# Optimization experiments

Hardware: AMD Instinct MI355X
Metric: run time of the kernel (lower is better)

Reference implementation:

```python
import jax, jax.numpy as jnp
import numpy as np


def sobel_kernels_3d(dtype=jnp.float32):
    # Standard 3D Sobel: derivative [-1,0,1] along one axis, smoothing [1,2,1]
    # along the other two. Returns shape (3, 1, 3, 3, 3) in OIDHW layout.
    s = jnp.array([1.0, 2.0, 1.0], dtype=dtype)
    d = jnp.array([-1.0, 0.0, 1.0], dtype=dtype)
    kd = jnp.einsum('i,j,k->ijk', d, s, s)  # d/dD
    kh = jnp.einsum('i,j,k->ijk', s, d, s)  # d/dH
    kw = jnp.einsum('i,j,k->ijk', s, s, d)  # d/dW
    return jnp.stack([kd, kh, kw], axis=0)[:, None]  # (3,1,3,3,3)


def _grad3d(x, kernels):
    # x: (B, C, D, H, W) -> flatten (B*C, 1, D, H, W), conv with padding=1.
    B, C, D, H, W = x.shape
    x_ = x.reshape(B * C, 1, D, H, W)
    return jax.lax.conv_general_dilated(
        x_, kernels.astype(x.dtype),
        window_strides=(1, 1, 1),
        padding=((1, 1), (1, 1), (1, 1)),
        dimension_numbers=('NCDHW', 'OIDHW', 'NCDHW'),
    )  # (B*C, 3, D, H, W)


def setup_inputs() -> dict:
    key = jax.random.key(0)
    k1, k2 = jax.random.split(key)
    shape = (4, 4, 64, 128, 128)
    pred = jax.random.normal(k1, shape, dtype=jnp.float32)
    target = jax.random.normal(k2, shape, dtype=jnp.float32)
    return {"pred": pred, "target": target}


def reference(pred, target):
    kernels = sobel_kernels_3d(pred.dtype)
    grad_pred = _grad3d(pred, kernels)
    grad_target = _grad3d(target, kernels)
    # loss_type == 'l1'
    return jnp.mean(jnp.abs(grad_pred - grad_target))
```

## Files before the change

### kernel.cpp

```cpp
#include <hip/hip_runtime.h>

#define NB 16
#define DD 64
#define HH 128
#define WW 128

constexpr int TH = 8;
constexpr int CD = 8;
constexpr int LY = TH + 2;
constexpr float INV_COUNT = 1.0f / 50331648.0f;

__global__ void zero_out_kernel(float* out) {
    if (threadIdx.x == 0 && blockIdx.x == 0) out[0] = 0.0f;
}

__global__ __launch_bounds__(256) void sobel_l1_kernel(
    const float* __restrict__ pred,
    const float* __restrict__ target,
    float* __restrict__ out)
{
    __shared__ float buf[2][LY * WW];
    __shared__ float wsum[4];

    const int tid = threadIdx.x;
    int b = blockIdx.x;
    const int bh = b & 15; b >>= 4;
    const int bc = b & 7;  b >>= 3;
    const int bn = b;

    const int h0 = bh * TH;
    const int d0 = bc * CD;
    const size_t nbase = (size_t)bn * (DD * HH * WW);

    const int tc  = tid & 31;
    const int lh  = tid >> 5;

    auto load_plane = [&](int gd, float4& v0, float4& v1) {
        v0 = float4{0.f, 0.f, 0.f, 0.f};
        v1 = float4{0.f, 0.f, 0.f, 0.f};
        if ((unsigned)gd < DD) {
            const size_t pbase = nbase + (size_t)gd * (HH * WW);
            const int gh = h0 - 1 + lh;
            if ((unsigned)gh < HH) {
                const size_t idx = pbase + (size_t)gh * WW + 4 * tc;
                const float4 p = *(const float4*)(pred + idx);
                const float4 q = *(const float4*)(target + idx);
                v0 = float4{p.x - q.x, p.y - q.y, p.z - q.z, p.w - q.w};
            }
            if (tid < 64) {
                const int gh2 = h0 - 1 + 8 + lh;
                if ((unsigned)gh2 < HH) {
                    const size_t idx = pbase + (size_t)gh2 * WW + 4 * tc;
                    const float4 p = *(const float4*)(pred + idx);
                    const float4 q = *(const float4*)(target + idx);
                    v1 = float4{p.x - q.x, p.y - q.y, p.z - q.z, p.w - q.w};
                }
            }
        }
    };

    auto store_plane = [&](int p, const float4& v0, const float4& v1) {
        float* B = buf[p];
        *(float4*)&B[lh * WW + 4 * tc] = v0;
        if (tid < 64)
            *(float4*)&B[(8 + lh) * WW + 4 * tc] = v1;
    };

    auto partial = [&](int p, float4& A_, float4& Bh_, float4& Bw_) {
        const float* B = buf[p];
        float4 rs[3], rdw[3];
#pragma unroll
        for (int r = 0; r < 3; ++r) {
            const float4 q = *(const float4*)&B[(lh + r) * WW + 4 * tc];
            float lm = __shfl_up(q.w, 1, 32);
            float rp = __shfl_down(q.x, 1, 32);
            if (tc == 0)  lm = 0.f;
            if (tc == 31) rp = 0.f;
            rs[r]  = float4{lm  + 2.f * q.x + q.y,
                            q.x + 2.f * q.y + q.z,
                            q.y + 2.f * q.z + q.w,
                            q.z + 2.f * q.w + rp};
            rdw[r] = float4{q.y - lm, q.z - q.x, q.w - q.y, rp - q.z};
        }
        A_  = float4{rs[0].x + 2.f * rs[1].x + rs[2].x,
                     rs[0].y + 2.f * rs[1].y + rs[2].y,
                     rs[0].z + 2.f * rs[1].z + rs[2].z,
                     rs[0].w + 2.f * rs[1].w + rs[2].w};
        Bh_ = float4{rs[2].x - rs[0].x, rs[2].y - rs[0].y,
                     rs[2].z - rs[0].z, rs[2].w - rs[0].w};
        Bw_ = float4{rdw[0].x + 2.f * rdw[1].x + rdw[2].x,
                     rdw[0].y + 2.f * rdw[1].y + rdw[2].y,
                     rdw[0].z + 2.f * rdw[1].z + rdw[2].z,
                     rdw[0].w + 2.f * rdw[1].w + rdw[2].w};
    };

    float4 rA[3], rBh[3], rBw[3];
    {
        float4 a0, a1, b0v, b1v;
        load_plane(d0 - 1, a0, a1);
        load_plane(d0,     b0v, b1v);
        store_plane(0, a0, a1);
        store_plane(1, b0v, b1v);
        __syncthreads();
        partial(0, rA[0], rBh[0], rBw[0]);
        partial(1, rA[1], rBh[1], rBw[1]);
    }

    float acc = 0.0f;
#pragma unroll
    for (int ld = 0; ld < CD; ++ld) {
        float4 c0, c1;
        load_plane(d0 + ld + 1, c0, c1);
        __syncthreads();
        store_plane(ld & 1, c0, c1);
        __syncthreads();
        const int s0 = ld % 3, s1 = (ld + 1) % 3, s2 = (ld + 2) % 3;
        partial(ld & 1, rA[s2], rBh[s2], rBw[s2]);

        const float4 a0 = rA[s0],  a2 = rA[s2];
        const float4 b0 = rBh[s0], b1 = rBh[s1], b2 = rBh[s2];
        const float4 c0v = rBw[s0], c1v = rBw[s1], c2v = rBw[s2];
        acc += fabsf(a2.x - a0.x) + fabsf(a2.y - a0.y)
             + fabsf(a2.z - a0.z) + fabsf(a2.w - a0.w);
        acc += fabsf(b0.x + 2.f * b1.x + b2.x) + fabsf(b0.y + 2.f * b1.y + b2.y)
             + fabsf(b0.z + 2.f * b1.z + b2.z) + fabsf(b0.w + 2.f * b1.w + b2.w);
        acc += fabsf(c0v.x + 2.f * c1v.x + c2v.x) + fabsf(c0v.y + 2.f * c1v.y + c2v.y)
             + fabsf(c0v.z + 2.f * c1v.z + c2v.z) + fabsf(c0v.w + 2.f * c1v.w + c2v.w);
    }

#pragma unroll
    for (int off = 32; off > 0; off >>= 1)
        acc += __shfl_down(acc, off, 64);
    const int wave = tid >> 6;
    if ((tid & 63) == 0) wsum[wave] = acc;
    __syncthreads();
    if (tid == 0) {
        const float s = wsum[0] + wsum[1] + wsum[2] + wsum[3];
        atomicAdd(out, s * INV_COUNT);
    }
}

extern "C" void kernel_launch(void* const* d_in, const int* in_sizes, int n_in,
                              void* d_out, int out_size, void* d_ws, size_t ws_size,
                              hipStream_t stream) {
    const float* pred   = (const float*)d_in[0];
    const float* target = (const float*)d_in[1];
    float* out = (float*)d_out;

    zero_out_kernel<<<1, 64, 0, stream>>>(out);

    const int nblocks = NB * (DD / CD) * (HH / TH);
    sobel_l1_kernel<<<nblocks, 256, 0, stream>>>(pred, target, out);
}
```

Measured before the change: 173.4 us.

## Drop shared-memory staging and read stencil rows straight from global memory

Removes the double-buffered shared-memory plane and the two __syncthreads per depth step. Each thread now loads its three H-rows of pred and target directly from global memory per plane, relying on L1/L2 to serve the overlapping rows between threads. This also sets launch bounds to 4 blocks per CU. The cost is roughly three times more global load instructions per plane, in exchange for no LDS traffic or block barriers and more latency hiding through occupancy.

New measurement: 206.2 us. 1.19x slower.

```diff
diff --git a/kernel.cpp b/kernel.cpp
--- a/kernel.cpp
+++ b/kernel.cpp
@@ -4,22 +4,21 @@
 #define DD 64
 #define HH 128
 #define WW 128
+#define HW (HH * WW)
 
 constexpr int TH = 8;
 constexpr int CD = 8;
-constexpr int LY = TH + 2;
 constexpr float INV_COUNT = 1.0f / 50331648.0f;
 
 __global__ void zero_out_kernel(float* out) {
     if (threadIdx.x == 0 && blockIdx.x == 0) out[0] = 0.0f;
 }
 
-__global__ __launch_bounds__(256) void sobel_l1_kernel(
+__global__ __launch_bounds__(256, 4) void sobel_l1_kernel(
     const float* __restrict__ pred,
     const float* __restrict__ target,
     float* __restrict__ out)
 {
-    __shared__ float buf[2][LY * WW];
     __shared__ float wsum[4];
 
     const int tid = threadIdx.x;
@@ -30,57 +29,43 @@
 
     const int h0 = bh * TH;
     const int d0 = bc * CD;
-    const size_t nbase = (size_t)bn * (DD * HH * WW);
+    const size_t nbase = (size_t)bn * (size_t)(DD * HW);
 
-    const int tc  = tid & 31;
-    const int lh  = tid >> 5;
+    const int tc = tid & 31;
+    const int lh = tid >> 5;
+    const int ghc = h0 + lh;
 
-    auto load_plane = [&](int gd, float4& v0, float4& v1) {
-        v0 = float4{0.f, 0.f, 0.f, 0.f};
-        v1 = float4{0.f, 0.f, 0.f, 0.f};
-        if ((unsigned)gd < DD) {
-            const size_t pbase = nbase + (size_t)gd * (HH * WW);
-            const int gh = h0 - 1 + lh;
-            if ((unsigned)gh < HH) {
-                const size_t idx = pbase + (size_t)gh * WW + 4 * tc;
-                const float4 p = *(const float4*)(pred + idx);
-                const float4 q = *(const float4*)(target + idx);
-                v0 = float4{p.x - q.x, p.y - q.y, p.z - q.z, p.w - q.w};
-            }
-            if (tid < 64) {
-                const int gh2 = h0 - 1 + 8 + lh;
-                if ((unsigned)gh2 < HH) {
-                    const size_t idx = pbase + (size_t)gh2 * WW + 4 * tc;
-                    const float4 p = *(const float4*)(pred + idx);
-                    const float4 q = *(const float4*)(target + idx);
-                    v1 = float4{p.x - q.x, p.y - q.y, p.z - q.z, p.w - q.w};
-                }
-            }
-        }
-    };
+    int  rowoff[3];
+    bool rowok[3];
+#pragma unroll
+    for (int r = 0; r < 3; ++r) {
+        const int gh = ghc - 1 + r;
+        rowok[r]  = (unsigned)gh < HH;
+        rowoff[r] = gh * WW + 4 * tc;
+    }
 
-    auto store_plane = [&](int p, const float4& v0, const float4& v1) {
-        float* B = buf[p];
-        *(float4*)&B[lh * WW + 4 * tc] = v0;
-        if (tid < 64)
-            *(float4*)&B[(8 + lh) * WW + 4 * tc] = v1;
-    };
-
-    auto partial = [&](int p, float4& A_, float4& Bh_, float4& Bw_) {
-        const float* B = buf[p];
+    auto plane_g = [&](int gd, float4& A_, float4& Bh_, float4& Bw_) {
+        const bool zok = (unsigned)gd < DD;
+        const size_t pb = nbase + (size_t)gd * HW;
         float4 rs[3], rdw[3];
 #pragma unroll
         for (int r = 0; r < 3; ++r) {
-            const float4 q = *(const float4*)&B[(lh + r) * WW + 4 * tc];
-            float lm = __shfl_up(q.w, 1, 32);
-            float rp = __shfl_down(q.x, 1, 32);
+            float4 v = float4{0.f, 0.f, 0.f, 0.f};
+            if (zok && rowok[r]) {
+                const size_t idx = pb + rowoff[r];
+                const float4 p = *(const float4*)(pred + idx);
+                const float4 q = *(const float4*)(target + idx);
+                v = float4{p.x - q.x, p.y - q.y, p.z - q.z, p.w - q.w};
+            }
+            float lm = __shfl_up(v.w, 1, 32);
+            float rp = __shfl_down(v.x, 1, 32);
             if (tc == 0)  lm = 0.f;
             if (tc == 31) rp = 0.f;
-            rs[r]  = float4{lm  + 2.f * q.x + q.y,
-                            q.x + 2.f * q.y + q.z,
-                            q.y + 2.f * q.z + q.w,
-                            q.z + 2.f * q.w + rp};
-            rdw[r] = float4{q.y - lm, q.z - q.x, q.w - q.y, rp - q.z};
+            rs[r]  = float4{lm  + 2.f * v.x + v.y,
+                            v.x + 2.f * v.y + v.z,
+                            v.y + 2.f * v.z + v.w,
+                            v.z + 2.f * v.w + rp};
+            rdw[r] = float4{v.y - lm, v.z - v.x, v.w - v.y, rp - v.z};
         }
         A_  = float4{rs[0].x + 2.f * rs[1].x + rs[2].x,
                      rs[0].y + 2.f * rs[1].y + rs[2].y,
@@ -95,37 +80,24 @@
     };
 
     float4 rA[3], rBh[3], rBw[3];
-    {
-        float4 a0, a1, b0v, b1v;
-        load_plane(d0 - 1, a0, a1);
-        load_plane(d0,     b0v, b1v);
-        store_plane(0, a0, a1);
-        store_plane(1, b0v, b1v);
-        __syncthreads();
-        partial(0, rA[0], rBh[0], rBw[0]);
-        partial(1, rA[1], rBh[1], rBw[1]);
-    }
+    plane_g(d0 - 1, rA[0], rBh[0], rBw[0]);
+    plane_g(d0,     rA[1], rBh[1], rBw[1]);
 
     float acc = 0.0f;
 #pragma unroll
     for (int ld = 0; ld < CD; ++ld) {
-        float4 c0, c1;
-        load_plane(d0 + ld + 1, c0, c1);
-        __syncthreads();
-        store_plane(ld & 1, c0, c1);
-        __syncthreads();
         const int s0 = ld % 3, s1 = (ld + 1) % 3, s2 = (ld + 2) % 3;
-        partial(ld & 1, rA[s2], rBh[s2], rBw[s2]);
+        plane_g(d0 + ld + 1, rA[s2], rBh[s2], rBw[s2]);
 
         const float4 a0 = rA[s0],  a2 = rA[s2];
         const float4 b0 = rBh[s0], b1 = rBh[s1], b2 = rBh[s2];
-        const float4 c0v = rBw[s0], c1v = rBw[s1], c2v = rBw[s2];
+        const float4 c0 = rBw[s0], c1 = rBw[s1], c2 = rBw[s2];
         acc += fabsf(a2.x - a0.x) + fabsf(a2.y - a0.y)
              + fabsf(a2.z - a0.z) + fabsf(a2.w - a0.w);
         acc += fabsf(b0.x + 2.f * b1.x + b2.x) + fabsf(b0.y + 2.f * b1.y + b2.y)
              + fabsf(b0.z + 2.f * b1.z + b2.z) + fabsf(b0.w + 2.f * b1.w + b2.w);
-        acc += fabsf(c0v.x + 2.f * c1v.x + c2v.x) + fabsf(c0v.y + 2.f * c1v.y + c2v.y)
-             + fabsf(c0v.z + 2.f * c1v.z + c2v.z) + fabsf(c0v.w + 2.f * c1v.w + c2v.w);
+        acc += fabsf(c0.x + 2.f * c1.x + c2.x) + fabsf(c0.y + 2.f * c1.y + c2.y)
+             + fabsf(c0.z + 2.f * c1.z + c2.z) + fabsf(c0.w + 2.f * c1.w + c2.w);
     }
 
 #pragma unroll
```
